# Kernel optimization log

Hardware: AMD Instinct MI355X
Metric: run time of the kernel (lower is better)

Reference implementation:

```python
import jax, jax.numpy as jnp
import numpy as np

EPS = 1e-05


def _convert(t):
    # torch: squeeze(0).permute(2,1,0): [1,C,H,W] -> [W,H,C]
    return jnp.transpose(t[0], (2, 1, 0))


def _histogram(t):
    # t: [W,H,C]; m: per-channel mean; h: [C, W*H]; ch: CxC covariance + eps*I
    m = t.mean(axis=(0, 1))
    c = t.shape[2]
    h = jnp.transpose(t - m, (2, 0, 1)).reshape(c, -1)
    ch = h @ h.T / h.shape[1] + EPS * jnp.eye(c, dtype=t.dtype)
    return m, h, ch


def _pca(c):
    # evec @ diag(sqrt(evals)) @ evec.T, with nan->0 on the sqrt
    w, v = jnp.linalg.eigh(c)
    e = jnp.sqrt(w)
    e = jnp.where(jnp.isnan(e), jnp.zeros_like(e), e)
    return (v * e[None, :]) @ v.T


def setup_inputs() -> dict:
    key = jax.random.key(0)
    k1, k2 = jax.random.split(key)
    shape = (1, 3, 2048, 2048)
    return {
        "input": jax.random.normal(k1, shape, dtype=jnp.float32),
        "source_tensor": jax.random.normal(k2, shape, dtype=jnp.float32),
    }


def reference(input, source_tensor):
    tgt = _convert(input)          # [W,H,C]
    src = _convert(source_tensor)  # [Ws,Hs,C]
    _, t, ct = _histogram(tgt)
    ms, _, cs = _histogram(src)
    # mode == 'pca': mt = pca(cs) @ inv(pca(ct)) @ t
    transform = _pca(cs) @ jnp.linalg.inv(_pca(ct))  # [C,C]
    mt = transform @ t                               # [C, W*H]
    w, h, c = tgt.shape
    matched = jnp.transpose(mt.reshape(c, w, h), (1, 2, 0)) + ms  # [W,H,C]
    # convert back: permute(2,1,0).unsqueeze(0) -> [1,C,H,W]
    return jnp.transpose(matched, (2, 1, 0))[None]
```

## Files before the change

kernel.cpp:

```cpp
#include <hip/hip_runtime.h>

#define EPS 1e-5
constexpr int BLOCK = 256;
constexpr int SBLOCKS = 1024;

__device__ void jacobi3(const double Ain[3][3], double w[3], double V[3][3]) {
    double A[3][3];
    for (int i = 0; i < 3; ++i)
        for (int j = 0; j < 3; ++j) {
            A[i][j] = Ain[i][j];
            V[i][j] = (i == j) ? 1.0 : 0.0;
        }
    const int pp[3] = {0, 0, 1};
    const int qq[3] = {1, 2, 2};
    for (int sweep = 0; sweep < 20; ++sweep) {
        double off = A[0][1]*A[0][1] + A[0][2]*A[0][2] + A[1][2]*A[1][2];
        if (off < 1e-28) break;
        for (int r3 = 0; r3 < 3; ++r3) {
            int p = pp[r3], q = qq[r3];
            double apq = A[p][q];
            if (apq == 0.0) continue;
            double theta = (A[q][q] - A[p][p]) / (2.0 * apq);
            double t = ((theta >= 0.0) ? 1.0 : -1.0) /
                       (fabs(theta) + sqrt(theta * theta + 1.0));
            double c = 1.0 / sqrt(t * t + 1.0);
            double s = t * c;
            A[p][p] -= t * apq;
            A[q][q] += t * apq;
            A[p][q] = A[q][p] = 0.0;
            int r = 3 - p - q;
            double arp = A[r][p], arq = A[r][q];
            A[r][p] = A[p][r] = c * arp - s * arq;
            A[r][q] = A[q][r] = s * arp + c * arq;
            for (int k = 0; k < 3; ++k) {
                double vkp = V[k][p], vkq = V[k][q];
                V[k][p] = c * vkp - s * vkq;
                V[k][q] = s * vkp + c * vkq;
            }
        }
    }
    w[0] = A[0][0]; w[1] = A[1][1]; w[2] = A[2][2];
}

__device__ void pca_pow(const double w[3], const double V[3][3], bool invert,
                        double P[3][3]) {
    double e[3];
    for (int k = 0; k < 3; ++k) {
        double ek = (w[k] > 0.0) ? sqrt(w[k]) : 0.0;
        if (invert) ek = (ek > 0.0) ? 1.0 / ek : 0.0;
        e[k] = ek;
    }
    for (int i = 0; i < 3; ++i)
        for (int j = 0; j < 3; ++j) {
            double t = 0;
            for (int k = 0; k < 3; ++k) t += V[i][k] * e[k] * V[j][k];
            P[i][j] = t;
        }
}

__device__ void solve_one(const double* a, double inv_n, bool invert,
                          double P[3][3], double mean[3]) {
    double m0 = a[0] * inv_n, m1 = a[1] * inv_n, m2 = a[2] * inv_n;
    mean[0] = m0; mean[1] = m1; mean[2] = m2;
    double C[3][3];
    C[0][0] = a[3] * inv_n - m0 * m0 + EPS;
    C[0][1] = C[1][0] = a[4] * inv_n - m0 * m1;
    C[0][2] = C[2][0] = a[5] * inv_n - m0 * m2;
    C[1][1] = a[6] * inv_n - m1 * m1 + EPS;
    C[1][2] = C[2][1] = a[7] * inv_n - m1 * m2;
    C[2][2] = a[8] * inv_n - m2 * m2 + EPS;
    double w[3], V[3][3];
    jacobi3(C, w, V);
    pca_pow(w, V, invert, P);
}

__device__ void combine_tb(const double Pt[3][3], const double Ps[3][3],
                           const double mt[3], const double ms[3],
                           float* tb) {
    double T[3][3];
    for (int i = 0; i < 3; ++i)
        for (int j = 0; j < 3; ++j) {
            double t = 0;
            for (int k = 0; k < 3; ++k) t += Ps[i][k] * Pt[k][j];
            T[i][j] = t;
        }
    for (int i = 0; i < 3; ++i) {
        double b = ms[i];
        for (int k = 0; k < 3; ++k) b -= T[i][k] * mt[k];
        tb[3 * i + 0] = (float)T[i][0];
        tb[3 * i + 1] = (float)T[i][1];
        tb[3 * i + 2] = (float)T[i][2];
        tb[9 + i] = (float)b;
    }
}

__global__ void stats_kernel(const float* __restrict__ in0,
                             const float* __restrict__ in1,
                             double* __restrict__ partials, int n4) {
    const int tid = threadIdx.x;
    const int lane = tid & 63;
    const int wid  = tid >> 6;
    const float4* base = (const float4*)(blockIdx.y ? in1 : in0);
    double s0 = 0, s1 = 0, s2 = 0;
    double q00 = 0, q01 = 0, q02 = 0, q11 = 0, q12 = 0, q22 = 0;
    const int stride = SBLOCKS * BLOCK;
    for (int i = blockIdx.x * BLOCK + tid; i < n4; i += stride) {
        float4 a = base[i];
        float4 b = base[i + n4];
        float4 c = base[i + 2 * n4];
#define ACC(f) { double x = (double)a.f, y = (double)b.f, z = (double)c.f;      \
        s0 += x; s1 += y; s2 += z;                                              \
        q00 = fma(x, x, q00); q01 = fma(x, y, q01); q02 = fma(x, z, q02);       \
        q11 = fma(y, y, q11); q12 = fma(y, z, q12); q22 = fma(z, z, q22); }
        ACC(x) ACC(y) ACC(z) ACC(w)
#undef ACC
    }
    double v[9] = {s0, s1, s2, q00, q01, q02, q11, q12, q22};
    __shared__ double sh[BLOCK / 64][9];
#pragma unroll
    for (int j = 0; j < 9; ++j) {
        double t = v[j];
#pragma unroll
        for (int o = 32; o > 0; o >>= 1) t += __shfl_down(t, o, 64);
        if (lane == 0) sh[wid][j] = t;
    }
    __syncthreads();
    if (tid == 0) {
        double* outp = partials + (blockIdx.y * SBLOCKS + blockIdx.x) * 9;
#pragma unroll
        for (int j = 0; j < 9; ++j)
            outp[j] = sh[0][j] + sh[1][j] + sh[2][j] + sh[3][j];
    }
}

__global__ void solve_kernel(const double* __restrict__ partials,
                             float* __restrict__ tb, double inv_n) {
    __shared__ double ssum[2][9];
    __shared__ double sP[2][3][3];
    __shared__ double sMean[2][3];
    __shared__ double sh[BLOCK / 64][9];
    const int tid = threadIdx.x;
    const int lane = tid & 63;
    const int wid  = tid >> 6;
    for (int im = 0; im < 2; ++im) {
        double v[9] = {0, 0, 0, 0, 0, 0, 0, 0, 0};
        for (int s = tid; s < SBLOCKS; s += BLOCK) {
            const double* p = partials + (im * SBLOCKS + s) * 9;
#pragma unroll
            for (int j = 0; j < 9; ++j) v[j] += p[j];
        }
#pragma unroll
        for (int j = 0; j < 9; ++j) {
            double t = v[j];
#pragma unroll
            for (int o = 32; o > 0; o >>= 1) t += __shfl_down(t, o, 64);
            if (lane == 0) sh[wid][j] = t;
        }
        __syncthreads();
        if (tid == 0) {
#pragma unroll
            for (int j = 0; j < 9; ++j)
                ssum[im][j] = sh[0][j] + sh[1][j] + sh[2][j] + sh[3][j];
        }
        __syncthreads();
    }
    if (tid < 2) {
        double P[3][3], mean[3];
        solve_one(ssum[tid], inv_n, tid == 0, P, mean);
        for (int i = 0; i < 3; ++i) {
            sMean[tid][i] = mean[i];
            for (int j = 0; j < 3; ++j) sP[tid][i][j] = P[i][j];
        }
    }
    __syncthreads();
    if (tid == 0) combine_tb(sP[0], sP[1], sMean[0], sMean[1], tb);
}

__global__ void apply_kernel(const float* __restrict__ in,
                             const float* __restrict__ tb,
                             float* __restrict__ out, int n4) {
    float t00 = tb[0], t01 = tb[1], t02 = tb[2];
    float t10 = tb[3], t11 = tb[4], t12 = tb[5];
    float t20 = tb[6], t21 = tb[7], t22 = tb[8];
    float b0 = tb[9], b1 = tb[10], b2 = tb[11];
    const float4* a = (const float4*)in;
    float4* o = (float4*)out;
    int stride = gridDim.x * blockDim.x;
    for (int i = blockIdx.x * blockDim.x + threadIdx.x; i < n4; i += stride) {
        float4 x = a[i];
        float4 y = a[i + n4];
        float4 z = a[i + 2 * n4];
        float4 r0, r1, r2;
#define AP(f) r0.f = fmaf(t00, x.f, fmaf(t01, y.f, fmaf(t02, z.f, b0)));       \
              r1.f = fmaf(t10, x.f, fmaf(t11, y.f, fmaf(t12, z.f, b1)));       \
              r2.f = fmaf(t20, x.f, fmaf(t21, y.f, fmaf(t22, z.f, b2)));
        AP(x) AP(y) AP(z) AP(w)
#undef AP
        o[i] = r0;
        o[i + n4] = r1;
        o[i + 2 * n4] = r2;
    }
}

extern "C" void kernel_launch(void* const* d_in, const int* in_sizes, int n_in,
                              void* d_out, int out_size, void* d_ws, size_t ws_size,
                              hipStream_t stream) {
    const float* in0 = (const float*)d_in[0];
    const float* in1 = (const float*)d_in[1];
    float* out = (float*)d_out;
    int total = in_sizes[0];
    int n = total / 3;
    int n4 = n / 4;

    double* partials = (double*)d_ws;
    float* tb = (float*)((char*)d_ws + 150528);
    double inv_n = 1.0 / (double)n;

    dim3 sgrid(SBLOCKS, 2);
    stats_kernel<<<sgrid, BLOCK, 0, stream>>>(in0, in1, partials, n4);
    solve_kernel<<<1, BLOCK, 0, stream>>>(partials, tb, inv_n);
    apply_kernel<<<2048, BLOCK, 0, stream>>>(in0, tb, out, n4);
}
```

Measured before the change: 56.56 us.

## Fuse solve into apply kernel, use fp32 stats accumulation, transpose partials layout

Every apply block now reduces the partials itself, solves the 3x3 PCA transform and computes the coefficients redundantly, which removes the separate single-block solve launch and its serial gap. The stats kernel accumulates per-thread sums in fp32 instead of fp64, cutting the cost of double-precision arithmetic, and partials are stored channel-major so the reduction loads are coalesced. In exchange, each of the 2048 blocks rereads the partials and runs the Jacobi solve, and fp32 per-thread accumulation loses some precision.

```diff
diff --git a/kernel.cpp b/kernel.cpp
--- a/kernel.cpp
+++ b/kernel.cpp
@@ -3,6 +3,7 @@
 #define EPS 1e-5
 constexpr int BLOCK = 256;
 constexpr int SBLOCKS = 1024;
+constexpr int NPART = SBLOCKS * 2;
 
 __device__ void jacobi3(const double Ain[3][3], double w[3], double V[3][3]) {
     double A[3][3];
@@ -101,21 +102,25 @@
     const int lane = tid & 63;
     const int wid  = tid >> 6;
     const float4* base = (const float4*)(blockIdx.y ? in1 : in0);
-    double s0 = 0, s1 = 0, s2 = 0;
-    double q00 = 0, q01 = 0, q02 = 0, q11 = 0, q12 = 0, q22 = 0;
+    float s0 = 0, s1 = 0, s2 = 0;
+    float q00 = 0, q01 = 0, q02 = 0, q11 = 0, q12 = 0, q22 = 0;
     const int stride = SBLOCKS * BLOCK;
+#define ACC1(x_, y_, z_) { float x = (x_), y = (y_), z = (z_);                  \
+        s0 += x; s1 += y; s2 += z;                                              \
+        q00 = fmaf(x, x, q00); q01 = fmaf(x, y, q01); q02 = fmaf(x, z, q02);    \
+        q11 = fmaf(y, y, q11); q12 = fmaf(y, z, q12); q22 = fmaf(z, z, q22); }
+#pragma unroll 2
     for (int i = blockIdx.x * BLOCK + tid; i < n4; i += stride) {
         float4 a = base[i];
         float4 b = base[i + n4];
         float4 c = base[i + 2 * n4];
-#define ACC(f) { double x = (double)a.f, y = (double)b.f, z = (double)c.f;      \
-        s0 += x; s1 += y; s2 += z;                                              \
-        q00 = fma(x, x, q00); q01 = fma(x, y, q01); q02 = fma(x, z, q02);       \
-        q11 = fma(y, y, q11); q12 = fma(y, z, q12); q22 = fma(z, z, q22); }
-        ACC(x) ACC(y) ACC(z) ACC(w)
-#undef ACC
-    }
-    double v[9] = {s0, s1, s2, q00, q01, q02, q11, q12, q22};
+        ACC1(a.x, b.x, c.x) ACC1(a.y, b.y, c.y)
+        ACC1(a.z, b.z, c.z) ACC1(a.w, b.w, c.w)
+    }
+#undef ACC1
+    double v[9] = {(double)s0, (double)s1, (double)s2,
+                   (double)q00, (double)q01, (double)q02,
+                   (double)q11, (double)q12, (double)q22};
     __shared__ double sh[BLOCK / 64][9];
 #pragma unroll
     for (int j = 0; j < 9; ++j) {
@@ -126,28 +131,36 @@
     }
     __syncthreads();
     if (tid == 0) {
-        double* outp = partials + (blockIdx.y * SBLOCKS + blockIdx.x) * 9;
+        const int g = blockIdx.y * SBLOCKS + blockIdx.x;
 #pragma unroll
         for (int j = 0; j < 9; ++j)
-            outp[j] = sh[0][j] + sh[1][j] + sh[2][j] + sh[3][j];
-    }
-}
-
-__global__ void solve_kernel(const double* __restrict__ partials,
-                             float* __restrict__ tb, double inv_n) {
+            partials[j * NPART + g] = sh[0][j] + sh[1][j] + sh[2][j] + sh[3][j];
+    }
+}
+
+__global__ __launch_bounds__(BLOCK, 4)
+void solve_apply_kernel(const float* __restrict__ in,
+                        const double* __restrict__ partials,
+                        float* __restrict__ out, int n4, double inv_n) {
+    const int tid = threadIdx.x;
+    const int lane = tid & 63;
+    const int wid  = tid >> 6;
+    __shared__ double sh[BLOCK / 64][9];
     __shared__ double ssum[2][9];
     __shared__ double sP[2][3][3];
     __shared__ double sMean[2][3];
-    __shared__ double sh[BLOCK / 64][9];
-    const int tid = threadIdx.x;
-    const int lane = tid & 63;
-    const int wid  = tid >> 6;
+    __shared__ float stb[12];
+
     for (int im = 0; im < 2; ++im) {
-        double v[9] = {0, 0, 0, 0, 0, 0, 0, 0, 0};
-        for (int s = tid; s < SBLOCKS; s += BLOCK) {
-            const double* p = partials + (im * SBLOCKS + s) * 9;
-#pragma unroll
-            for (int j = 0; j < 9; ++j) v[j] += p[j];
+        double v[9];
+#pragma unroll
+        for (int j = 0; j < 9; ++j) {
+            double t = 0;
+            const double* p = partials + j * NPART + im * SBLOCKS;
+#pragma unroll
+            for (int s = 0; s < SBLOCKS / BLOCK; ++s)
+                t += p[s * BLOCK + tid];
+            v[j] = t;
         }
 #pragma unroll
         for (int j = 0; j < 9; ++j) {
@@ -164,6 +177,7 @@
         }
         __syncthreads();
     }
+
     if (tid < 2) {
         double P[3][3], mean[3];
         solve_one(ssum[tid], inv_n, tid == 0, P, mean);
@@ -173,27 +187,24 @@
         }
     }
     __syncthreads();
-    if (tid == 0) combine_tb(sP[0], sP[1], sMean[0], sMean[1], tb);
-}
-
-__global__ void apply_kernel(const float* __restrict__ in,
-                             const float* __restrict__ tb,
-                             float* __restrict__ out, int n4) {
-    float t00 = tb[0], t01 = tb[1], t02 = tb[2];
-    float t10 = tb[3], t11 = tb[4], t12 = tb[5];
-    float t20 = tb[6], t21 = tb[7], t22 = tb[8];
-    float b0 = tb[9], b1 = tb[10], b2 = tb[11];
+    if (tid == 0) combine_tb(sP[0], sP[1], sMean[0], sMean[1], stb);
+    __syncthreads();
+
+    const float t00 = stb[0], t01 = stb[1], t02 = stb[2];
+    const float t10 = stb[3], t11 = stb[4], t12 = stb[5];
+    const float t20 = stb[6], t21 = stb[7], t22 = stb[8];
+    const float b0 = stb[9], b1 = stb[10], b2 = stb[11];
     const float4* a = (const float4*)in;
     float4* o = (float4*)out;
-    int stride = gridDim.x * blockDim.x;
-    for (int i = blockIdx.x * blockDim.x + threadIdx.x; i < n4; i += stride) {
+    const int stride = gridDim.x * BLOCK;
+    for (int i = blockIdx.x * BLOCK + tid; i < n4; i += stride) {
         float4 x = a[i];
         float4 y = a[i + n4];
         float4 z = a[i + 2 * n4];
         float4 r0, r1, r2;
 #define AP(f) r0.f = fmaf(t00, x.f, fmaf(t01, y.f, fmaf(t02, z.f, b0)));       \
               r1.f = fmaf(t10, x.f, fmaf(t11, y.f, fmaf(t12, z.f, b1)));       \
-              r2.f = fmaf(t20, x.f, fmaf(t21, y.f, fmaf(t22, z.f, b2)));
+              r2.f = fmaf(t20, x.f, fmaf(t22, z.f, fmaf(t21, y.f, b2)));
         AP(x) AP(y) AP(z) AP(w)
 #undef AP
         o[i] = r0;
@@ -213,11 +224,9 @@
     int n4 = n / 4;
 
     double* partials = (double*)d_ws;
-    float* tb = (float*)((char*)d_ws + 150528);
     double inv_n = 1.0 / (double)n;
 
     dim3 sgrid(SBLOCKS, 2);
     stats_kernel<<<sgrid, BLOCK, 0, stream>>>(in0, in1, partials, n4);
-    solve_kernel<<<1, BLOCK, 0, stream>>>(partials, tb, inv_n);
-    apply_kernel<<<2048, BLOCK, 0, stream>>>(in0, tb, out, n4);
-}
+    solve_apply_kernel<<<2048, BLOCK, 0, stream>>>(in0, partials, out, n4, inv_n);
+}
```

New measurement: 62.88 us. 11.2% more time.
